# Performance work log

Hardware: AMD Instinct MI355X
Metric: run time of the kernel (lower is better)

## Reference

```python
import jax, jax.numpy as jnp
import numpy as np

B, S, IN, H, NC, WSEG = 2, 256, 80, 128, 40, 64
F2 = 2 * H  # bidirectional LSTM output dim


def setup_inputs() -> dict:
    key = jax.random.key(0)
    it = iter(jax.random.split(key, 48))
    def nrm(shape, scale):
        return jax.random.normal(next(it), shape, jnp.float32) * scale
    d = {}
    d["x"] = jax.random.normal(next(it), (B, S, IN), jnp.float32)
    d["lengths"] = jnp.full((B,), S, dtype=jnp.int32)
    ins = [IN, F2]
    for l in range(2):
        for dr in ("f", "b"):
            sc = 1.0 / np.sqrt(H)
            d[f"w_ih_l{l}{dr}"] = nrm((4 * H, ins[l]), sc)
            d[f"w_hh_l{l}{dr}"] = nrm((4 * H, H), sc)
            d[f"b_l{l}{dr}"] = nrm((4 * H,), sc)
    PD = 3 * F2  # pairwise phi feature dim
    d["a_s0"] = jnp.float32(0.25); d["w_s1"] = nrm((100, PD), 1.0 / np.sqrt(PD)); d["b_s1"] = jnp.zeros((100,), jnp.float32)
    d["a_s1"] = jnp.float32(0.25); d["w_s2"] = nrm((1, 100), 0.1); d["b_s2"] = jnp.zeros((1,), jnp.float32)
    d["a_c0"] = jnp.float32(0.25); d["w_c1"] = nrm((2 * NC, F2), 1.0 / np.sqrt(F2)); d["b_c1"] = jnp.zeros((2 * NC,), jnp.float32)
    d["a_c1"] = jnp.float32(0.25); d["w_c2"] = nrm((NC, 2 * NC), 0.1); d["b_c2"] = jnp.zeros((NC,), jnp.float32)
    d["a_b0"] = jnp.float32(0.25); d["w_b1"] = nrm((2 * NC, F2), 1.0 / np.sqrt(F2)); d["b_b1"] = jnp.zeros((2 * NC,), jnp.float32)
    d["a_b1"] = jnp.float32(0.25); d["w_b2"] = nrm((2, 2 * NC), 0.1); d["b_b2"] = jnp.zeros((2,), jnp.float32)
    return d


def prelu(x, a):
    return jnp.where(x >= 0, x, a * x)


def mlp(x, a0, W1, b1, a1, W2, b2):
    h = prelu(x, a0) @ W1.T + b1
    return prelu(h, a1) @ W2.T + b2


def lstm_dir(x, Wih, Whh, b, reverse):
    # PyTorch gate order: i, f, g, o
    pre = jnp.einsum("bsi,gi->sbg", x, Wih) + b  # [S,B,4H]
    if reverse:
        pre = pre[::-1]
    h0 = jnp.zeros((x.shape[0], Whh.shape[1]), x.dtype)
    def step(carry, xt):
        h, c = carry
        g = xt + h @ Whh.T
        i, f, gg, o = jnp.split(g, 4, axis=-1)
        c = jax.nn.sigmoid(f) * c + jax.nn.sigmoid(i) * jnp.tanh(gg)
        h = jax.nn.sigmoid(o) * jnp.tanh(c)
        return (h, c), h
    _, hs = jax.lax.scan(step, (h0, h0), pre)
    if reverse:
        hs = hs[::-1]
    return jnp.swapaxes(hs, 0, 1)  # [B,S,H]


def encode(x, layers):
    out = x
    for (wif, whf, bf, wib, whb, bb) in layers:
        out = jnp.concatenate([
            lstm_dir(out, wif, whf, bf, False),
            lstm_dir(out, wib, whb, bb, True),
        ], axis=-1)
    return out


def compute_scores(rnn_out, a_s0, w_s1, b_s1, a_s1, w_s2, b_s2):
    cum = jnp.cumsum(rnn_out, axis=1)
    # phi[b,i,j] = [cum[j]-cum[i], out[i], out[j]]  (faithful to calc_phi)
    c = cum[:, None, :, :] - cum[:, :, None, :]
    sh = c.shape
    dmat = jnp.broadcast_to(rnn_out[:, :, None, :], sh)
    emat = jnp.broadcast_to(rnn_out[:, None, :, :], sh)
    phi = jnp.concatenate([c, dmat, emat], axis=-1)  # [B,S,S,3*F2]
    return mlp(phi, a_s0, w_s1, b_s1, a_s1, w_s2, b_s2)[..., 0]  # [B,S,S]


def dp_backptr(scores):
    # Viterbi-style DP: best[i] = max_{j in [i-WSEG, i)} best[j] + scores[:, j, i]
    Bn, Sn = scores.shape[:2]
    def step(best, i):
        start = jnp.maximum(0, i - WSEG)
        jidx = start + jnp.arange(WSEG)
        bwin = jax.lax.dynamic_slice(best, (0, start), (Bn, WSEG))
        swin = jax.lax.dynamic_slice(scores, (0, start, i), (Bn, WSEG, 1))[..., 0]
        cand = jnp.where(jidx[None, :] < i, bwin + swin, -1e9)
        k = (start + jnp.argmax(cand, axis=1)).astype(jnp.int32)
        best = jax.lax.dynamic_update_slice(best, jnp.max(cand, axis=1, keepdims=True), (0, i))
        return best, k
    _, ks = jax.lax.scan(step, jnp.zeros((Bn, Sn), scores.dtype), jnp.arange(1, Sn))
    backptr = jnp.concatenate([jnp.zeros((1, Bn), jnp.int32), ks], axis=0).T  # [B,S]
    return backptr


def backtrack(scores, backptr, lengths):
    Bn, Sn = scores.shape[:2]
    bar = jnp.arange(Bn)
    def step(carry, _):
        cur, acc, bm = carry
        bm = bm.at[bar, cur].set(True)
        prev = backptr[bar, cur]
        active = cur > 0
        acc = acc + jnp.where(active, scores[bar, prev, cur], 0.0)
        cur = jnp.where(active, prev, 0)
        return (cur, acc, bm), None
    init = ((lengths - 1).astype(jnp.int32), jnp.zeros((Bn,), scores.dtype), jnp.zeros((Bn, Sn), bool))
    (_, acc, bm), _ = jax.lax.scan(step, init, None, length=Sn)
    return bm, acc


def reference(x, lengths,
              w_ih_l0f, w_hh_l0f, b_l0f, w_ih_l0b, w_hh_l0b, b_l0b,
              w_ih_l1f, w_hh_l1f, b_l1f, w_ih_l1b, w_hh_l1b, b_l1b,
              a_s0, w_s1, b_s1, a_s1, w_s2, b_s2,
              a_c0, w_c1, b_c1, a_c1, w_c2, b_c2,
              a_b0, w_b1, b_b1, a_b1, w_b2, b_b2):
    layers = [
        (w_ih_l0f, w_hh_l0f, b_l0f, w_ih_l0b, w_hh_l0b, b_l0b),
        (w_ih_l1f, w_hh_l1f, b_l1f, w_ih_l1b, w_hh_l1b, b_l1b),
    ]
    rnn_out = encode(x, layers)  # [B,S,2H]
    cls_out = mlp(rnn_out, a_c0, w_c1, b_c1, a_c1, w_c2, b_c2)
    bin_out = mlp(rnn_out, a_b0, w_b1, b_b1, a_b1, w_b2, b_b2)
    scores = compute_scores(rnn_out, a_s0, w_s1, b_s1, a_s1, w_s2, b_s2)
    backptr = dp_backptr(scores)
    bmask, pred_scores = backtrack(scores, backptr, lengths)
    # bmask[b,i]==1 iff i is a predicted segment boundary (padded-dense encoding of pred lists)
    return cls_out, bin_out, bmask.astype(jnp.int32), pred_scores
```

## Files before the change

### kernel.cpp

```cpp
#include <hip/hip_runtime.h>
#include <math.h>


#define OFF_BIN 20480
#define OFF_BM  21504
#define OFF_PRED 22016

__device__ __forceinline__ float preluf(float x, float a) { return x >= 0.f ? x : a * x; }
__device__ __forceinline__ float sigf(float x) { return 1.f / (1.f + __expf(-x)); }
__device__ __forceinline__ float tanh_fast(float x) { return 1.f - 2.f / (__expf(2.f * x) + 1.f); }

__global__ __launch_bounds__(256) void k_gemm(const float* __restrict__ A,
                                              const float* __restrict__ B,
                                              int Adim, int K,
                                              const float* __restrict__ wf,
                                              const float* __restrict__ bf,
                                              const float* __restrict__ wb,
                                              const float* __restrict__ bbv,
                                              float* __restrict__ outF,
                                              float* __restrict__ outB) {
    int mtile = blockIdx.y;
    int dir = mtile >> 3;
    const float* W = dir ? wb : wf;
    const float* bias = dir ? bbv : bf;
    float* out = dir ? outB : outF;
    int g0 = (mtile & 7) << 6;
    int tb0 = blockIdx.x << 6;
    int tid = threadIdx.x;
    int Bdim = K - Adim;

    __shared__ float Ws[16][68];
    __shared__ float Xs[16][68];

    int r = tid >> 2, c4 = tid & 3;
    int tbr = tb0 + r;
    int hr = ((tbr & 1) << 8) | (tbr >> 1);
    int ty = tid >> 4;
    int tx = tid & 15;
    float acc[4][4] = {};

    for (int k0 = 0; k0 < K; k0 += 16) {
        float4 wv = *(const float4*)(W + (size_t)(g0 + r) * K + k0 + (c4 << 2));
        const float* src = (k0 < Adim) ? (A + (size_t)hr * Adim + k0)
                                       : (B + (size_t)hr * Bdim + (k0 - Adim));
        float4 xv = *(const float4*)(src + (c4 << 2));
        __syncthreads();
        int kc = c4 << 2;
        Ws[kc + 0][r] = wv.x; Ws[kc + 1][r] = wv.y; Ws[kc + 2][r] = wv.z; Ws[kc + 3][r] = wv.w;
        Xs[kc + 0][r] = xv.x; Xs[kc + 1][r] = xv.y; Xs[kc + 2][r] = xv.z; Xs[kc + 3][r] = xv.w;
        __syncthreads();
#pragma unroll
        for (int kk = 0; kk < 16; ++kk) {
            float4 wq = *(const float4*)&Ws[kk][ty << 2];
            float4 xq = *(const float4*)&Xs[kk][tx << 2];
            acc[0][0] += wq.x * xq.x; acc[0][1] += wq.x * xq.y; acc[0][2] += wq.x * xq.z; acc[0][3] += wq.x * xq.w;
            acc[1][0] += wq.y * xq.x; acc[1][1] += wq.y * xq.y; acc[1][2] += wq.y * xq.z; acc[1][3] += wq.y * xq.w;
            acc[2][0] += wq.z * xq.x; acc[2][1] += wq.z * xq.y; acc[2][2] += wq.z * xq.z; acc[2][3] += wq.z * xq.w;
            acc[3][0] += wq.w * xq.x; acc[3][1] += wq.w * xq.y; acc[3][2] += wq.w * xq.z; acc[3][3] += wq.w * xq.w;
        }
    }
    int gq = g0 + (ty << 2);
    float b0 = bias[gq], b1 = bias[gq + 1], b2 = bias[gq + 2], b3 = bias[gq + 3];
#pragma unroll
    for (int j = 0; j < 4; ++j) {
        int tb = tb0 + (tx << 2) + j;
        float4 v = make_float4(acc[0][j] + b0, acc[1][j] + b1, acc[2][j] + b2, acc[3][j] + b3);
        *(float4*)(out + (size_t)tb * 512 + gq) = v;
    }
}

__global__ __launch_bounds__(512, 2) void k_lstm(const float* __restrict__ pre_f,
                                                 const float* __restrict__ pre_b,
                                                 const float* __restrict__ whh_f,
                                                 const float* __restrict__ whh_b,
                                                 float* __restrict__ hout_f,
                                                 float* __restrict__ hout_b) {
    const int dir = blockIdx.x >> 1;
    const int b = blockIdx.x & 1;
    const float* pre = dir ? pre_b : pre_f;
    const float* whh = dir ? whh_b : whh_f;
    float* hout = dir ? hout_b : hout_f;
    const int tid = threadIdx.x;
    const int c = tid >> 7;
    const int gg = tid & 127;
    const int k0 = c << 5;

    float w[4][32];
#pragma unroll
    for (int j = 0; j < 4; ++j) {
#pragma unroll
        for (int k = 0; k < 32; k += 4) {
            float4 v = *(const float4*)(whh + (size_t)((j << 7) + gg) * 128 + k0 + k);
            w[j][k] = v.x; w[j][k + 1] = v.y; w[j][k + 2] = v.z; w[j][k + 3] = v.w;
        }
    }

    __shared__ __align__(16) float hl[128];
    __shared__ float4 part[4][128];
    if (tid < 128) hl[tid] = 0.f;
    float cst = 0.f;
    __syncthreads();

    int t0 = dir ? 255 : 0;
    const float* pp0 = pre + ((size_t)t0 * 2 + b) * 512;
    float p0 = pp0[gg], p1 = pp0[128 + gg], p2 = pp0[256 + gg], p3 = pp0[384 + gg];

    for (int step = 0; step < 256; ++step) {
        int t = dir ? (255 - step) : step;
        float n0 = 0.f, n1 = 0.f, n2 = 0.f, n3 = 0.f;
        if (step < 255) {
            int tn = dir ? (254 - step) : (step + 1);
            const float* pp = pre + ((size_t)tn * 2 + b) * 512;
            n0 = pp[gg]; n1 = pp[128 + gg]; n2 = pp[256 + gg]; n3 = pp[384 + gg];
        }
        float a0 = 0.f, a1 = 0.f, a2 = 0.f, a3 = 0.f;
#pragma unroll
        for (int k = 0; k < 32; k += 4) {
            float4 h4 = *(const float4*)(hl + k0 + k);
            a0 += w[0][k] * h4.x + w[0][k + 1] * h4.y + w[0][k + 2] * h4.z + w[0][k + 3] * h4.w;
            a1 += w[1][k] * h4.x + w[1][k + 1] * h4.y + w[1][k + 2] * h4.z + w[1][k + 3] * h4.w;
            a2 += w[2][k] * h4.x + w[2][k + 1] * h4.y + w[2][k + 2] * h4.z + w[2][k + 3] * h4.w;
            a3 += w[3][k] * h4.x + w[3][k + 1] * h4.y + w[3][k + 2] * h4.z + w[3][k + 3] * h4.w;
        }
        part[c][gg] = make_float4(a0, a1, a2, a3);
        __syncthreads();
        float4 q0 = part[0][gg], q1 = part[1][gg], q2 = part[2][gg], q3 = part[3][gg];
        float gi = p0 + ((q0.x + q1.x) + (q2.x + q3.x));
        float gf = p1 + ((q0.y + q1.y) + (q2.y + q3.y));
        float gG = p2 + ((q0.z + q1.z) + (q2.z + q3.z));
        float go = p3 + ((q0.w + q1.w) + (q2.w + q3.w));
        cst = sigf(gf) * cst + sigf(gi) * tanh_fast(gG);
        float h = sigf(go) * tanh_fast(cst);
        hl[gg] = h;
        if (tid < 128) hout[(size_t)(((b << 8) + t) << 7) + gg] = h;
        p0 = n0; p1 = n1; p2 = n2; p3 = n3;
        __syncthreads();
    }
}

__global__ __launch_bounds__(256) void k_feats(const float* __restrict__ h1f,
                                               const float* __restrict__ h1b,
                                               const float* __restrict__ ws1,
                                               const float* __restrict__ bs1,
                                               const float* a_s0,
                                               float* __restrict__ Pd,
                                               float* __restrict__ Pe,
                                               const float* ac0p, const float* __restrict__ wc1,
                                               const float* __restrict__ bc1, const float* ac1p,
                                               const float* __restrict__ wc2, const float* __restrict__ bc2,
                                               const float* ab0p, const float* __restrict__ wb1,
                                               const float* __restrict__ bb1, const float* ab1p,
                                               const float* __restrict__ wb2, const float* __restrict__ bb2,
                                               float* __restrict__ out,
                                               float* __restrict__ cum) {
    __shared__ __align__(16) float xa[256];
    __shared__ __align__(16) float xb2[256];
    __shared__ __align__(16) float hc[80];
    __shared__ __align__(16) float hb[80];
    int bid = blockIdx.x;
    int tid = threadIdx.x;
    int kk = tid & 127;
    if (bid < 512) {
        int row = bid;
        float a0 = a_s0[0];
        float v = ((tid < 128) ? h1f : h1b)[(size_t)row * 128 + kk];
        xa[tid] = preluf(v, a0);
        __syncthreads();
        const float4* p4 = (const float4*)xa;
        if (tid < 100) {
            const float4* wr = (const float4*)(ws1 + (size_t)tid * 768 + 256);
            float acc = bs1[tid];
#pragma unroll 8
            for (int q = 0; q < 64; ++q) {
                float4 w4 = wr[q], x4 = p4[q];
                acc += w4.x * x4.x + w4.y * x4.y + w4.z * x4.z + w4.w * x4.w;
            }
            Pd[(size_t)row * 100 + tid] = acc;
        } else if (tid >= 128 && tid < 228) {
            int u = tid - 128;
            const float4* wr = (const float4*)(ws1 + (size_t)u * 768 + 512);
            float acc = 0.f;
#pragma unroll 8
            for (int q = 0; q < 64; ++q) {
                float4 w4 = wr[q], x4 = p4[q];
                acc += w4.x * x4.x + w4.y * x4.y + w4.z * x4.z + w4.w * x4.w;
            }
            Pe[(size_t)row * 100 + u] = acc;
        }
    } else if (bid < 1024) {
        int row = bid - 512;
        float ac0 = ac0p[0], ac1 = ac1p[0], ab0 = ab0p[0], ab1 = ab1p[0];
        float v = ((tid < 128) ? h1f : h1b)[(size_t)row * 128 + kk];
        xa[tid] = preluf(v, ac0);
        xb2[tid] = preluf(v, ab0);
        __syncthreads();
        if (tid < 80) {
            const float4* wr = (const float4*)(wc1 + (size_t)tid * 256);
            const float4* x4 = (const float4*)xa;
            float acc = bc1[tid];
#pragma unroll 8
            for (int q = 0; q < 64; ++q) {
                float4 w4 = wr[q], p = x4[q];
                acc += w4.x * p.x + w4.y * p.y + w4.z * p.z + w4.w * p.w;
            }
            hc[tid] = preluf(acc, ac1);
        } else if (tid >= 128 && tid < 208) {
            int u = tid - 128;
            const float4* wr = (const float4*)(wb1 + (size_t)u * 256);
            const float4* x4 = (const float4*)xb2;
            float acc = bb1[u];
#pragma unroll 8
            for (int q = 0; q < 64; ++q) {
                float4 w4 = wr[q], p = x4[q];
                acc += w4.x * p.x + w4.y * p.y + w4.z * p.z + w4.w * p.w;
            }
            hb[u] = preluf(acc, ab1);
        }
        __syncthreads();
        if (tid < 40) {
            const float4* wr = (const float4*)(wc2 + (size_t)tid * 80);
            const float4* h4 = (const float4*)hc;
            float acc = bc2[tid];
#pragma unroll
            for (int q = 0; q < 20; ++q) {
                float4 w4 = wr[q], p = h4[q];
                acc += w4.x * p.x + w4.y * p.y + w4.z * p.z + w4.w * p.w;
            }
            out[(size_t)row * 40 + tid] = acc;
        } else if (tid >= 64 && tid < 66) {
            int j = tid - 64;
            const float4* wr = (const float4*)(wb2 + (size_t)j * 80);
            const float4* h4 = (const float4*)hb;
            float acc = bb2[j];
#pragma unroll
            for (int q = 0; q < 20; ++q) {
                float4 w4 = wr[q], p = h4[q];
                acc += w4.x * p.x + w4.y * p.y + w4.z * p.z + w4.w * p.w;
            }
            out[OFF_BIN + (size_t)row * 2 + j] = acc;
        }
    } else {
        int b = bid - 1024;
        const float* src = (tid < 128) ? h1f : h1b;
        float run = 0.f;
#pragma unroll 8
        for (int t = 0; t < 256; ++t) {
            float v = src[(size_t)(((b << 8) + t) << 7) + kk];
            cum[(size_t)(((b << 8) + t) << 8) + tid] = run + v;
            run += v;
        }
    }
}

__global__ __launch_bounds__(256) void k_scores(const float* __restrict__ cum,
                                                const float* __restrict__ ws1,
                                                const float* __restrict__ ws2,
                                                const float* __restrict__ bs2,
                                                const float* __restrict__ Pd,
                                                const float* __restrict__ Pe,
                                                const float* a_s0p, const float* a_s1p,
                                                float* __restrict__ scT) {
    int bid = blockIdx.x;
    int dt = bid & 3, et = (bid >> 2) & 127, b = bid >> 9;
    int d0 = dt << 6, e0 = et << 1;
    int tid = threadIdx.x;
    __shared__ float cumd[64][260];
    __shared__ __align__(16) float cume[2][260];
    __shared__ float red[4][2][64];
    float a0 = a_s0p[0], a1 = a_s1p[0];
    {
        int r = tid >> 2, q = tid & 3;
        const float4* src = (const float4*)(cum + (size_t)(((b << 8) + (d0 + r)) << 8) + (q << 6));
        float4* dst = (float4*)&cumd[r][q << 6];
#pragma unroll
        for (int x = 0; x < 16; ++x) dst[x] = src[x];
    }
    if (tid < 128) {
        int er = tid >> 6, kq = tid & 63;
        float4 v = *((const float4*)(cum + (size_t)(((b << 8) + (e0 + er)) << 8)) + kq);
        *((float4*)&cume[er][0] + kq) = v;
    }
    __syncthreads();

    int ug = __builtin_amdgcn_readfirstlane(tid >> 6);
    int ld = tid & 63;
    float acc0[25], acc1[25];
#pragma unroll
    for (int t = 0; t < 25; ++t) { acc0[t] = 0.f; acc1[t] = 0.f; }
    const float* wc = ws1 + (size_t)(ug * 25) * 768;
    for (int k = 0; k < 256; k += 4) {
        float4 cd = *(const float4*)&cumd[ld][k];
        float4 c0 = *(const float4*)&cume[0][k];
        float4 c1 = *(const float4*)&cume[1][k];
        float4 y0, y1;
        y0.x = preluf(c0.x - cd.x, a0); y0.y = preluf(c0.y - cd.y, a0);
        y0.z = preluf(c0.z - cd.z, a0); y0.w = preluf(c0.w - cd.w, a0);
        y1.x = preluf(c1.x - cd.x, a0); y1.y = preluf(c1.y - cd.y, a0);
        y1.z = preluf(c1.z - cd.z, a0); y1.w = preluf(c1.w - cd.w, a0);
#pragma unroll
        for (int t = 0; t < 25; ++t) {
            float4 wq = *(const float4*)(wc + (size_t)t * 768 + k);
            acc0[t] += y0.x * wq.x + y0.y * wq.y + y0.z * wq.z + y0.w * wq.w;
            acc1[t] += y1.x * wq.x + y1.y * wq.y + y1.z * wq.z + y1.w * wq.w;
        }
    }
    const float* pdrow = Pd + (size_t)((b << 8) + d0 + ld) * 100;
    {
        const float* perow = Pe + (size_t)((b << 8) + e0) * 100;
        float part = 0.f;
#pragma unroll
        for (int t = 0; t < 25; ++t) {
            int u = ug * 25 + t;
            float h = acc0[t] + pdrow[u] + perow[u];
            part += preluf(h, a1) * ws2[u];
        }
        red[ug][0][ld] = part;
    }
    {
        const float* perow = Pe + (size_t)((b << 8) + e0 + 1) * 100;
        float part = 0.f;
#pragma unroll
        for (int t = 0; t < 25; ++t) {
            int u = ug * 25 + t;
            float h = acc1[t] + pdrow[u] + perow[u];
            part += preluf(h, a1) * ws2[u];
        }
        red[ug][1][ld] = part;
    }
    __syncthreads();
    if (tid < 128) {
        int e = tid >> 6, l2 = tid & 63;
        float s = red[0][e][l2] + red[1][e][l2] + red[2][e][l2] + red[3][e][l2] + bs2[0];
        scT[(size_t)(((b << 8) + (e0 + e)) << 8) + d0 + l2] = s;
    }
}

__device__ __forceinline__ void argmax_dpp(float& v, int& ki) {
#define AD_STEP(CTRL, RMASK)                                                                    \
    {                                                                                           \
        int mv = __builtin_amdgcn_update_dpp(__float_as_int(v), __float_as_int(v), CTRL, RMASK, 0xf, false); \
        int mk = __builtin_amdgcn_update_dpp(ki, ki, CTRL, RMASK, 0xf, false);                  \
        float fv = __int_as_float(mv);                                                          \
        bool take = (fv > v) || (fv == v && mk < ki);                                           \
        v = take ? fv : v;                                                                      \
        ki = take ? mk : ki;                                                                    \
    }
    AD_STEP(0x111, 0xf)
    AD_STEP(0x112, 0xf)
    AD_STEP(0x114, 0xf)
    AD_STEP(0x118, 0xf)
    AD_STEP(0x142, 0xa)
    AD_STEP(0x143, 0xc)
#undef AD_STEP
}

__global__ __launch_bounds__(128) void k_dp(const float* __restrict__ scT,
                                            const int* __restrict__ lengths,
                                            float* __restrict__ out) {
    __shared__ int bp[2][256];
    __shared__ float bm[2][256];
    int tid = threadIdx.x;
    for (int i = tid; i < 512; i += 128) {
        ((int*)bp)[i] = 0;
        ((float*)bm)[i] = 0.f;
    }
    __syncthreads();
    int b = tid >> 6, ln = tid & 63;
    const float* sb = scT + ((size_t)b << 16);
    int lenm1 = lengths[b] - 1;
    float wreg = 0.f;
    float bestFinal = 0.f;
    int jcur = (ln < 1) ? ln : ln - 64;
    float sc_next = sb[(1 << 8) + ((jcur < 0) ? 0 : jcur)];
    for (int i = 1; i < 256; ++i) {
        float sc = sc_next;
        int j = jcur;
        if (i < 255) {
            int m2 = (i + 1) & 63;
            int base2 = (i + 1) - m2;
            int j2 = (ln < m2) ? (base2 + ln) : (base2 + ln - 64);
            jcur = j2;
            sc_next = sb[((i + 1) << 8) + ((j2 < 0) ? 0 : j2)];
        }
        float v = (j >= 0) ? (wreg + sc) : -1000000000.0f;
        int ki = j;
        argmax_dpp(v, ki);
        float bv = __uint_as_float(__builtin_amdgcn_readlane(__float_as_uint(v), 63));
        int bk = __builtin_amdgcn_readlane(ki, 63);
        if (ln == (i & 63)) wreg = bv;
        if (ln == 0) bp[b][i] = bk;
        if (i == lenm1) bestFinal = bv;
    }
    if (ln == 0) out[OFF_PRED + b] = bestFinal;
    __syncthreads();
    if (tid < 2) {
        int bb = tid;
        int cur = lengths[bb] - 1;
        for (int it = 0; it < 256; ++it) {
            bm[bb][cur] = 1.f;
            int prev = bp[bb][cur];
            cur = (cur > 0) ? prev : 0;
        }
    }
    __syncthreads();
    for (int i = tid; i < 512; i += 128) out[OFF_BM + i] = ((float*)bm)[i];
}

extern "C" void kernel_launch(void* const* d_in, const int* in_sizes, int n_in,
                              void* d_out, int out_size, void* d_ws, size_t ws_size,
                              hipStream_t stream) {
    const float* x     = (const float*)d_in[0];
    const int* lengths = (const int*)d_in[1];
    const float* wih0f = (const float*)d_in[2];
    const float* whh0f = (const float*)d_in[3];
    const float* b0f   = (const float*)d_in[4];
    const float* wih0b = (const float*)d_in[5];
    const float* whh0b = (const float*)d_in[6];
    const float* b0b   = (const float*)d_in[7];
    const float* wih1f = (const float*)d_in[8];
    const float* whh1f = (const float*)d_in[9];
    const float* b1f   = (const float*)d_in[10];
    const float* wih1b = (const float*)d_in[11];
    const float* whh1b = (const float*)d_in[12];
    const float* b1b   = (const float*)d_in[13];
    const float* a_s0  = (const float*)d_in[14];
    const float* w_s1  = (const float*)d_in[15];
    const float* b_s1  = (const float*)d_in[16];
    const float* a_s1  = (const float*)d_in[17];
    const float* w_s2  = (const float*)d_in[18];
    const float* b_s2  = (const float*)d_in[19];
    const float* a_c0  = (const float*)d_in[20];
    const float* w_c1  = (const float*)d_in[21];
    const float* b_c1  = (const float*)d_in[22];
    const float* a_c1  = (const float*)d_in[23];
    const float* w_c2  = (const float*)d_in[24];
    const float* b_c2  = (const float*)d_in[25];
    const float* a_b0  = (const float*)d_in[26];
    const float* w_b1  = (const float*)d_in[27];
    const float* b_b1  = (const float*)d_in[28];
    const float* a_b1  = (const float*)d_in[29];
    const float* w_b2  = (const float*)d_in[30];
    const float* b_b2  = (const float*)d_in[31];

    float* wsf = (float*)d_ws;
    float* preF = wsf;
    float* preB = wsf + 262144;
    float* h0f  = wsf + 524288;
    float* h0b  = wsf + 589824;
    float* h1f  = wsf + 655360;
    float* h1b  = wsf + 720896;
    float* cum  = wsf + 786432;
    float* Pd   = wsf + 917504;
    float* Pe   = wsf + 968704;
    float* scT  = wsf + 1019904;
    float* out  = (float*)d_out;

    k_gemm<<<dim3(8, 16), 256, 0, stream>>>(x, x, 80, 80, wih0f, b0f, wih0b, b0b, preF, preB);
    k_lstm<<<4, 512, 0, stream>>>(preF, preB, whh0f, whh0b, h0f, h0b);
    k_gemm<<<dim3(8, 16), 256, 0, stream>>>(h0f, h0b, 128, 256, wih1f, b1f, wih1b, b1b, preF, preB);
    k_lstm<<<4, 512, 0, stream>>>(preF, preB, whh1f, whh1b, h1f, h1b);
    k_feats<<<1026, 256, 0, stream>>>(h1f, h1b, w_s1, b_s1, a_s0, Pd, Pe,
                                      a_c0, w_c1, b_c1, a_c1, w_c2, b_c2,
                                      a_b0, w_b1, b_b1, a_b1, w_b2, b_b2, out, cum);
    k_scores<<<1024, 256, 0, stream>>>(cum, w_s1, w_s2, b_s2, Pd, Pe, a_s0, a_s1, scT);
    k_dp<<<1, 128, 0, stream>>>(scT, lengths, out);
}
```

Measured before the change: 1.068 ms.

## Process four e-rows per block in pairwise scores kernel to reuse weight loads

```diff
diff --git a/kernel.cpp b/kernel.cpp
--- a/kernel.cpp
+++ b/kernel.cpp
@@ -252,83 +252,86 @@
     }
 }
 
-__global__ __launch_bounds__(256) void k_scores(const float* __restrict__ cum,
-                                                const float* __restrict__ ws1,
-                                                const float* __restrict__ ws2,
-                                                const float* __restrict__ bs2,
-                                                const float* __restrict__ Pd,
-                                                const float* __restrict__ Pe,
-                                                const float* a_s0p, const float* a_s1p,
-                                                float* __restrict__ scT) {
+__global__ __launch_bounds__(256, 2) void k_scores(const float* __restrict__ cum,
+                                                   const float* __restrict__ ws1,
+                                                   const float* __restrict__ ws2,
+                                                   const float* __restrict__ bs2,
+                                                   const float* __restrict__ Pd,
+                                                   const float* __restrict__ Pe,
+                                                   const float* a_s0p, const float* a_s1p,
+                                                   float* __restrict__ scT) {
     int bid = blockIdx.x;
-    int dt = bid & 3, et = (bid >> 2) & 127, b = bid >> 9;
-    int d0 = dt << 6, e0 = et << 1;
+    int dt = bid & 3, et = (bid >> 2) & 63, b = bid >> 8;
+    int d0 = dt << 6, e0 = et << 2;
     int tid = threadIdx.x;
-    __shared__ float cumd[64][260];
-    __shared__ __align__(16) float cume[2][260];
-    __shared__ float red[4][2][64];
+    __shared__ float cumd[64][257];
+    __shared__ float cume[4][257];
+    __shared__ float red[4][4][64];
     float a0 = a_s0p[0], a1 = a_s1p[0];
+
     {
-        int r = tid >> 2, q = tid & 3;
-        const float4* src = (const float4*)(cum + (size_t)(((b << 8) + (d0 + r)) << 8) + (q << 6));
-        float4* dst = (float4*)&cumd[r][q << 6];
-#pragma unroll
-        for (int x = 0; x < 16; ++x) dst[x] = src[x];
-    }
-    if (tid < 128) {
-        int er = tid >> 6, kq = tid & 63;
-        float4 v = *((const float4*)(cum + (size_t)(((b << 8) + (e0 + er)) << 8)) + kq);
-        *((float4*)&cume[er][0] + kq) = v;
+        int rowd = tid & 63, w = tid >> 6;
+        const float4* src = (const float4*)(cum + (size_t)(((b << 8) + (d0 + rowd)) << 8) + (w << 6));
+        float* dst = &cumd[rowd][w << 6];
+#pragma unroll
+        for (int x = 0; x < 16; ++x) {
+            float4 v = src[x];
+            dst[(x << 2) + 0] = v.x; dst[(x << 2) + 1] = v.y;
+            dst[(x << 2) + 2] = v.z; dst[(x << 2) + 3] = v.w;
+        }
+    }
+    {
+        int er = tid >> 6, j = tid & 63;
+        float4 v = *((const float4*)(cum + (size_t)(((b << 8) + (e0 + er)) << 8)) + j);
+        float* dst = &cume[er][j << 2];
+        dst[0] = v.x; dst[1] = v.y; dst[2] = v.z; dst[3] = v.w;
     }
     __syncthreads();
 
     int ug = __builtin_amdgcn_readfirstlane(tid >> 6);
     int ld = tid & 63;
-    float acc0[25], acc1[25];
-#pragma unroll
-    for (int t = 0; t < 25; ++t) { acc0[t] = 0.f; acc1[t] = 0.f; }
+    float acc0[25], acc1[25], acc2[25], acc3[25];
+#pragma unroll
+    for (int t = 0; t < 25; ++t) { acc0[t] = 0.f; acc1[t] = 0.f; acc2[t] = 0.f; acc3[t] = 0.f; }
     const float* wc = ws1 + (size_t)(ug * 25) * 768;
+
     for (int k = 0; k < 256; k += 4) {
-        float4 cd = *(const float4*)&cumd[ld][k];
-        float4 c0 = *(const float4*)&cume[0][k];
-        float4 c1 = *(const float4*)&cume[1][k];
-        float4 y0, y1;
-        y0.x = preluf(c0.x - cd.x, a0); y0.y = preluf(c0.y - cd.y, a0);
-        y0.z = preluf(c0.z - cd.z, a0); y0.w = preluf(c0.w - cd.w, a0);
-        y1.x = preluf(c1.x - cd.x, a0); y1.y = preluf(c1.y - cd.y, a0);
-        y1.z = preluf(c1.z - cd.z, a0); y1.w = preluf(c1.w - cd.w, a0);
+        float cd0 = cumd[ld][k], cd1 = cumd[ld][k + 1], cd2 = cumd[ld][k + 2], cd3 = cumd[ld][k + 3];
+        float4 y0 = make_float4(preluf(cume[0][k] - cd0, a0), preluf(cume[0][k + 1] - cd1, a0),
+                                preluf(cume[0][k + 2] - cd2, a0), preluf(cume[0][k + 3] - cd3, a0));
+        float4 y1 = make_float4(preluf(cume[1][k] - cd0, a0), preluf(cume[1][k + 1] - cd1, a0),
+                                preluf(cume[1][k + 2] - cd2, a0), preluf(cume[1][k + 3] - cd3, a0));
+        float4 y2 = make_float4(preluf(cume[2][k] - cd0, a0), preluf(cume[2][k + 1] - cd1, a0),
+                                preluf(cume[2][k + 2] - cd2, a0), preluf(cume[2][k + 3] - cd3, a0));
+        float4 y3 = make_float4(preluf(cume[3][k] - cd0, a0), preluf(cume[3][k + 1] - cd1, a0),
+                                preluf(cume[3][k + 2] - cd2, a0), preluf(cume[3][k + 3] - cd3, a0));
 #pragma unroll
         for (int t = 0; t < 25; ++t) {
             float4 wq = *(const float4*)(wc + (size_t)t * 768 + k);
             acc0[t] += y0.x * wq.x + y0.y * wq.y + y0.z * wq.z + y0.w * wq.w;
             acc1[t] += y1.x * wq.x + y1.y * wq.y + y1.z * wq.z + y1.w * wq.w;
-        }
-    }
+            acc2[t] += y2.x * wq.x + y2.y * wq.y + y2.z * wq.z + y2.w * wq.w;
+            acc3[t] += y3.x * wq.x + y3.y * wq.y + y3.z * wq.z + y3.w * wq.w;
+        }
+    }
+
     const float* pdrow = Pd + (size_t)((b << 8) + d0 + ld) * 100;
+#define EPI(ACC, EE)                                                      \
+    {                                                                     \
+        const float* perow = Pe + (size_t)((b << 8) + e0 + EE) * 100;     \
+        float part = 0.f;                                                 \
+        _Pragma("unroll")                                                 \
+        for (int t = 0; t < 25; ++t) {                                    \
+            int u = ug * 25 + t;                                          \
+            float h = ACC[t] + pdrow[u] + perow[u];                       \
+            part += preluf(h, a1) * ws2[u];                               \
+        }                                                                 \
+        red[ug][EE][ld] = part;                                           \
+    }
+    EPI(acc0, 0) EPI(acc1, 1) EPI(acc2, 2) EPI(acc3, 3)
+#undef EPI
+    __syncthreads();
     {
-        const float* perow = Pe + (size_t)((b << 8) + e0) * 100;
-        float part = 0.f;
-#pragma unroll
-        for (int t = 0; t < 25; ++t) {
-            int u = ug * 25 + t;
-            float h = acc0[t] + pdrow[u] + perow[u];
-            part += preluf(h, a1) * ws2[u];
-        }
-        red[ug][0][ld] = part;
-    }
-    {
-        const float* perow = Pe + (size_t)((b << 8) + e0 + 1) * 100;
-        float part = 0.f;
-#pragma unroll
-        for (int t = 0; t < 25; ++t) {
-            int u = ug * 25 + t;
-            float h = acc1[t] + pdrow[u] + perow[u];
-            part += preluf(h, a1) * ws2[u];
-        }
-        red[ug][1][ld] = part;
-    }
-    __syncthreads();
-    if (tid < 128) {
         int e = tid >> 6, l2 = tid & 63;
         float s = red[0][e][l2] + red[1][e][l2] + red[2][e][l2] + red[3][e][l2] + bs2[0];
         scT[(size_t)(((b << 8) + (e0 + e)) << 8) + d0 + l2] = s;
@@ -462,6 +465,6 @@
     k_feats<<<1026, 256, 0, stream>>>(h1f, h1b, w_s1, b_s1, a_s0, Pd, Pe,
                                       a_c0, w_c1, b_c1, a_c1, w_c2, b_c2,
                                       a_b0, w_b1, b_b1, a_b1, w_b2, b_b2, out, cum);
-    k_scores<<<1024, 256, 0, stream>>>(cum, w_s1, w_s2, b_s2, Pd, Pe, a_s0, a_s1, scT);
+    k_scores<<<512, 256, 0, stream>>>(cum, w_s1, w_s2, b_s2, Pd, Pe, a_s0, a_s1, scT);
     k_dp<<<1, 128, 0, stream>>>(scT, lengths, out);
 }
```

After: 1.039 ms. -2.6%, faster.

## Retile pairwise score kernel to 32x4 d/e tiles with smaller shared memory

Applied to the files above, without the earlier changes.

```diff
diff --git a/kernel.cpp b/kernel.cpp
--- a/kernel.cpp
+++ b/kernel.cpp
@@ -252,61 +252,69 @@
     }
 }
 
-__global__ __launch_bounds__(256) void k_scores(const float* __restrict__ cum,
-                                                const float* __restrict__ ws1,
-                                                const float* __restrict__ ws2,
-                                                const float* __restrict__ bs2,
-                                                const float* __restrict__ Pd,
-                                                const float* __restrict__ Pe,
-                                                const float* a_s0p, const float* a_s1p,
-                                                float* __restrict__ scT) {
+__global__ __launch_bounds__(256, 4) void k_scores(const float* __restrict__ cum,
+                                                   const float* __restrict__ ws1,
+                                                   const float* __restrict__ ws2,
+                                                   const float* __restrict__ bs2,
+                                                   const float* __restrict__ Pd,
+                                                   const float* __restrict__ Pe,
+                                                   const float* a_s0p, const float* a_s1p,
+                                                   float* __restrict__ scT) {
     int bid = blockIdx.x;
-    int dt = bid & 3, et = (bid >> 2) & 127, b = bid >> 9;
-    int d0 = dt << 6, e0 = et << 1;
+    int dt = bid & 7, et = (bid >> 3) & 63, b = bid >> 9;
+    int d0 = dt << 5, e0 = et << 2;
     int tid = threadIdx.x;
-    __shared__ float cumd[64][260];
-    __shared__ __align__(16) float cume[2][260];
-    __shared__ float red[4][2][64];
+    __shared__ float cumd[32][257];
+    __shared__ float cume[4][257];
+    __shared__ float red[4][4][32];
     float a0 = a_s0p[0], a1 = a_s1p[0];
+
     {
-        int r = tid >> 2, q = tid & 3;
-        const float4* src = (const float4*)(cum + (size_t)(((b << 8) + (d0 + r)) << 8) + (q << 6));
-        float4* dst = (float4*)&cumd[r][q << 6];
-#pragma unroll
-        for (int x = 0; x < 16; ++x) dst[x] = src[x];
-    }
-    if (tid < 128) {
-        int er = tid >> 6, kq = tid & 63;
-        float4 v = *((const float4*)(cum + (size_t)(((b << 8) + (e0 + er)) << 8)) + kq);
-        *((float4*)&cume[er][0] + kq) = v;
+        int r = tid & 31, w = tid >> 5;
+        const float4* src = (const float4*)(cum + (size_t)(((b << 8) + (d0 + r)) << 8) + (w << 5));
+        float* dst = &cumd[r][w << 5];
+#pragma unroll
+        for (int x = 0; x < 8; ++x) {
+            float4 v = src[x];
+            dst[(x << 2) + 0] = v.x; dst[(x << 2) + 1] = v.y;
+            dst[(x << 2) + 2] = v.z; dst[(x << 2) + 3] = v.w;
+        }
+    }
+    {
+        int er = tid >> 6, j = tid & 63;
+        float4 v = *((const float4*)(cum + (size_t)(((b << 8) + (e0 + er)) << 8)) + j);
+        float* dst = &cume[er][j << 2];
+        dst[0] = v.x; dst[1] = v.y; dst[2] = v.z; dst[3] = v.w;
     }
     __syncthreads();
 
     int ug = __builtin_amdgcn_readfirstlane(tid >> 6);
-    int ld = tid & 63;
+    int lane = tid & 63;
+    int dd = lane & 31;
+    int eh = lane >> 5;
+    int ea = (eh << 1), ebn = ea + 1;
     float acc0[25], acc1[25];
 #pragma unroll
     for (int t = 0; t < 25; ++t) { acc0[t] = 0.f; acc1[t] = 0.f; }
     const float* wc = ws1 + (size_t)(ug * 25) * 768;
+
     for (int k = 0; k < 256; k += 4) {
-        float4 cd = *(const float4*)&cumd[ld][k];
-        float4 c0 = *(const float4*)&cume[0][k];
-        float4 c1 = *(const float4*)&cume[1][k];
-        float4 y0, y1;
-        y0.x = preluf(c0.x - cd.x, a0); y0.y = preluf(c0.y - cd.y, a0);
-        y0.z = preluf(c0.z - cd.z, a0); y0.w = preluf(c0.w - cd.w, a0);
-        y1.x = preluf(c1.x - cd.x, a0); y1.y = preluf(c1.y - cd.y, a0);
-        y1.z = preluf(c1.z - cd.z, a0); y1.w = preluf(c1.w - cd.w, a0);
+        float cd0 = cumd[dd][k], cd1 = cumd[dd][k + 1], cd2 = cumd[dd][k + 2], cd3 = cumd[dd][k + 3];
+        float4 ya = make_float4(preluf(cume[ea][k] - cd0, a0), preluf(cume[ea][k + 1] - cd1, a0),
+                                preluf(cume[ea][k + 2] - cd2, a0), preluf(cume[ea][k + 3] - cd3, a0));
+        float4 yb = make_float4(preluf(cume[ebn][k] - cd0, a0), preluf(cume[ebn][k + 1] - cd1, a0),
+                                preluf(cume[ebn][k + 2] - cd2, a0), preluf(cume[ebn][k + 3] - cd3, a0));
 #pragma unroll
         for (int t = 0; t < 25; ++t) {
             float4 wq = *(const float4*)(wc + (size_t)t * 768 + k);
-            acc0[t] += y0.x * wq.x + y0.y * wq.y + y0.z * wq.z + y0.w * wq.w;
-            acc1[t] += y1.x * wq.x + y1.y * wq.y + y1.z * wq.z + y1.w * wq.w;
-        }
-    }
-    const float* pdrow = Pd + (size_t)((b << 8) + d0 + ld) * 100;
+            acc0[t] += ya.x * wq.x + ya.y * wq.y + ya.z * wq.z + ya.w * wq.w;
+            acc1[t] += yb.x * wq.x + yb.y * wq.y + yb.z * wq.z + yb.w * wq.w;
+        }
+    }
+
+    const float* pdrow = Pd + (size_t)((b << 8) + d0 + dd) * 100;
     {
-        const float* perow = Pe + (size_t)((b << 8) + e0) * 100;
+        const float* perow = Pe + (size_t)((b << 8) + e0 + ea) * 100;
         float part = 0.f;
 #pragma unroll
         for (int t = 0; t < 25; ++t) {
@@ -314,10 +322,10 @@
             float h = acc0[t] + pdrow[u] + perow[u];
             part += preluf(h, a1) * ws2[u];
         }
-        red[ug][0][ld] = part;
+        red[ug][ea][dd] = part;
     }
     {
-        const float* perow = Pe + (size_t)((b << 8) + e0 + 1) * 100;
+        const float* perow = Pe + (size_t)((b << 8) + e0 + ebn) * 100;
         float part = 0.f;
 #pragma unroll
         for (int t = 0; t < 25; ++t) {
@@ -325,11 +333,11 @@
             float h = acc1[t] + pdrow[u] + perow[u];
             part += preluf(h, a1) * ws2[u];
         }
-        red[ug][1][ld] = part;
+        red[ug][ebn][dd] = part;
     }
     __syncthreads();
     if (tid < 128) {
-        int e = tid >> 6, l2 = tid & 63;
+        int e = tid >> 5, l2 = tid & 31;
         float s = red[0][e][l2] + red[1][e][l2] + red[2][e][l2] + red[3][e][l2] + bs2[0];
         scT[(size_t)(((b << 8) + (e0 + e)) << 8) + d0 + l2] = s;
     }
```

New measurement: 957.5 us. -10.3%, faster.
